# Optimization experiments

Hardware: AMD Instinct MI355X
Metric: run time of the kernel (lower is better)

Reference implementation:

```python
import jax, jax.numpy as jnp
import numpy as np

T, S, B, D, H, FFN = 1024, 1024, 4, 1024, 16, 4096
HD = D // H
EPS = 1e-5


def xavier(key, shape, gain=1.0):
    fan_out, fan_in = shape
    a = gain * np.sqrt(6.0 / (fan_in + fan_out))
    return jax.random.uniform(key, shape, jnp.float32, -a, a)


def layer_norm(x, g, b):
    mu = jnp.mean(x, axis=-1, keepdims=True)
    var = jnp.mean(jnp.square(x - mu), axis=-1, keepdims=True)
    return (x - mu) / jnp.sqrt(var + EPS) * g + b


def mha(q, k, v, Wq, bq, Wk, bk, Wv, bv, Wo, bo, key_padding_mask=None, attn_mask=None):
    # q: [t,b,d]; k,v: [s,b,d]; key_padding_mask: [b,s] bool (True = pad)
    t, b, d = q.shape
    s = v.shape[0]
    if key_padding_mask is not None:
        # original zeroes the KEY tensor before projection
        k = k * (~key_padding_mask).T[:, :, None]
    Q = (q @ Wq.T + bq).reshape(t, b, H, HD)
    K = (k @ Wk.T + bk).reshape(s, b, H, HD)
    V = (v @ Wv.T + bv).reshape(s, b, H, HD)
    scores = jnp.einsum('tbhk,sbhk->bhts', Q, K) / jnp.sqrt(jnp.float32(HD))
    if attn_mask is not None:
        scores = scores + attn_mask  # additive [t,s] broadcast over b,h
    p = jax.nn.softmax(scores, axis=-1)
    ctx = jnp.einsum('bhts,sbhk->tbhk', p, V)  # [t,b,h,hd]
    out = ctx.reshape(t, b, d)
    attn_w = jnp.swapaxes(ctx, 0, 2)  # [h,b,t,hd] as in original
    return out @ Wo.T + bo, attn_w


def setup_inputs() -> dict:
    key = jax.random.key(0)
    ks = jax.random.split(key, 16)
    inv2 = 1.0 / np.sqrt(2.0)
    d = {
        'state': jax.random.normal(ks[0], (T, B, D), jnp.float32),
        'encoder_out': jax.random.normal(ks[1], (S, B, D), jnp.float32),
        'self_attn_mask': jnp.triu(jnp.full((T, T), -1e9, jnp.float32), 1),
        'self_attn_padding_mask': jnp.zeros((B, T), bool),
        'encoder_padding_mask': jnp.broadcast_to(jnp.arange(S)[None, :] >= (S - S // 10), (B, S)),
        # self-attention projections
        'sa_Wq': xavier(ks[2], (D, D), inv2), 'sa_bq': jnp.zeros((D,), jnp.float32),
        'sa_Wk': xavier(ks[3], (D, D), inv2), 'sa_bk': jnp.zeros((D,), jnp.float32),
        'sa_Wv': xavier(ks[4], (D, D), inv2), 'sa_bv': jnp.zeros((D,), jnp.float32),
        'sa_Wo': xavier(ks[5], (D, D)), 'sa_bo': jnp.zeros((D,), jnp.float32),
        # encoder-decoder attention projections
        'ea_Wq': xavier(ks[6], (D, D), inv2), 'ea_bq': jnp.zeros((D,), jnp.float32),
        'ea_Wk': xavier(ks[7], (D, D), inv2), 'ea_bk': jnp.zeros((D,), jnp.float32),
        'ea_Wv': xavier(ks[8], (D, D), inv2), 'ea_bv': jnp.zeros((D,), jnp.float32),
        'ea_Wo': xavier(ks[9], (D, D)), 'ea_bo': jnp.zeros((D,), jnp.float32),
        # layernorms
        'ln1_g': jnp.ones((D,), jnp.float32), 'ln1_b': jnp.zeros((D,), jnp.float32),
        'ln2_g': jnp.ones((D,), jnp.float32), 'ln2_b': jnp.zeros((D,), jnp.float32),
        'ln3_g': jnp.ones((D,), jnp.float32), 'ln3_b': jnp.zeros((D,), jnp.float32),
        # FFN
        'fc1_W': xavier(ks[10], (FFN, D)), 'fc1_b': jnp.zeros((FFN,), jnp.float32),
        'fc2_W': xavier(ks[11], (D, FFN)), 'fc2_b': jnp.zeros((D,), jnp.float32),
    }
    return d


def reference(state, encoder_out, self_attn_mask, self_attn_padding_mask, encoder_padding_mask,
              sa_Wq, sa_bq, sa_Wk, sa_bk, sa_Wv, sa_bv, sa_Wo, sa_bo,
              ea_Wq, ea_bq, ea_Wk, ea_bk, ea_Wv, ea_bv, ea_Wo, ea_bo,
              ln1_g, ln1_b, ln2_g, ln2_b, ln3_g, ln3_b,
              fc1_W, fc1_b, fc2_W, fc2_b):
    x = state
    # self-attention block (dropout is identity in eval)
    res = x
    a, _ = mha(x, x, x, sa_Wq, sa_bq, sa_Wk, sa_bk, sa_Wv, sa_bv, sa_Wo, sa_bo,
               key_padding_mask=self_attn_padding_mask, attn_mask=self_attn_mask)
    x = layer_norm(a + res, ln1_g, ln1_b)
    # encoder-decoder attention block
    res = x
    a, attn = mha(x, encoder_out, encoder_out, ea_Wq, ea_bq, ea_Wk, ea_bk, ea_Wv, ea_bv, ea_Wo, ea_bo,
                  key_padding_mask=encoder_padding_mask, attn_mask=None)
    x = layer_norm(a + res, ln2_g, ln2_b)
    # FFN block
    res = x
    h = jax.nn.relu(x @ fc1_W.T + fc1_b)
    x = layer_norm(h @ fc2_W.T + fc2_b + res, ln3_g, ln3_b)
    return (x, attn)
```

## Files before the change

kernel.cpp:

```cpp
#include <hip/hip_runtime.h>
#include <hip/hip_bf16.h>


typedef __attribute__((ext_vector_type(8))) short bf16x8;
typedef __attribute__((ext_vector_type(4))) float f32x4;
typedef __attribute__((ext_vector_type(8))) unsigned short us8;
typedef __attribute__((ext_vector_type(4))) unsigned short us4;

#define AS1 __attribute__((address_space(1)))
#define AS3 __attribute__((address_space(3)))

#define T_LEN 1024
#define S_LEN 1024
#define B_DIM 4
#define D_MOD 1024
#define H_NUM 16
#define FFN_D 4096
#define NTOK  4096

__device__ __forceinline__ float b2f(unsigned short u) {
    return __uint_as_float(((unsigned int)u) << 16);
}
__device__ __forceinline__ unsigned short f2b(float f) {
    unsigned int x = __float_as_uint(f);
    x += 0x7fffu + ((x >> 16) & 1u);
    return (unsigned short)(x >> 16);
}

struct CvtArgs {
    const float* s[12];
    unsigned short* d[12];
};

__global__ __launch_bounds__(256) void cvt_all_kernel(CvtArgs a)
{
    const int cnt[12] = {2048, 2048, 512, 512, 512, 512, 512, 512, 512, 512, 2048, 2048};
    int bid = blockIdx.x;
    int seg = 0;
    while (bid >= cnt[seg]) { bid -= cnt[seg]; ++seg; }
    const size_t off = (size_t)bid * 2048 + threadIdx.x * 8;
    const float* src = a.s[seg] + off;
    unsigned short* dst = a.d[seg] + off;
    const f32x4 v0 = *(const f32x4*)src;
    const f32x4 v1 = *(const f32x4*)(src + 4);
    us8 o;
#pragma unroll
    for (int j = 0; j < 4; ++j) { o[j] = f2b(v0[j]); o[4 + j] = f2b(v1[j]); }
    *(us8*)dst = o;
}

template <int BN>
__global__ __launch_bounds__(512, 2) void gemm256_kernel(
    const unsigned short* __restrict__ A,
    const unsigned short* __restrict__ W,
    const float* __restrict__ b0, const float* __restrict__ b1,
    const float* __restrict__ b2, const float* __restrict__ b3,
    const int* __restrict__ rowmask, unsigned int maskbits,
    unsigned short* __restrict__ p0, unsigned short* __restrict__ p1,
    unsigned short* __restrict__ p2, unsigned short* __restrict__ p3,
    int ostride,
    const float* __restrict__ resid, float* __restrict__ outf,
    int M, int N, int K, int relu)
{
    constexpr int WN = BN / 4;
    constexpr int NR = BN / 64;

    __shared__ __align__(16) unsigned short As[2][16384];
    __shared__ __align__(16) unsigned short Bs[2][BN * 64];

    const int tid  = threadIdx.x;
    const int lane = tid & 63;
    const int wid  = tid >> 6;
    const int wr   = wid >> 2;
    const int wc   = wid & 3;
    const int row0 = blockIdx.x * 256;
    const int col0 = blockIdx.y * BN;
    const int rsel = lane & 15;
    const int kg2  = (lane >> 4) * 16;

    f32x4 acc[8][NR];
#pragma unroll
    for (int m = 0; m < 8; ++m)
#pragma unroll
        for (int n = 0; n < NR; ++n)
            acc[m][n] = (f32x4){0.f, 0.f, 0.f, 0.f};

    const int NT = K >> 6;

    auto stage = [&](int buf, int t) {
        const int k0 = t << 6;
#pragma unroll
        for (int i = 0; i < 4; ++i) {
            const unsigned int beta = (unsigned int)(i * 8192 + tid * 16);
            const unsigned int lam  = beta ^ (((beta >> 7) & 7u) << 4);
            const char* src = (const char*)A +
                ((size_t)(row0 + (int)(lam >> 7)) * K + k0) * 2 + (lam & 127u);
            __builtin_amdgcn_global_load_lds((const AS1 void*)src,
                (AS3 void*)((char*)&As[buf][0] + beta), 16, 0, 0);
        }
#pragma unroll
        for (int i = 0; i < NR; ++i) {
            const unsigned int beta = (unsigned int)(i * 8192 + tid * 16);
            const unsigned int lam  = beta ^ (((beta >> 7) & 7u) << 4);
            const char* src = (const char*)W +
                ((size_t)(col0 + (int)(lam >> 7)) * K + k0) * 2 + (lam & 127u);
            __builtin_amdgcn_global_load_lds((const AS1 void*)src,
                (AS3 void*)((char*)&Bs[buf][0] + beta), 16, 0, 0);
        }
    };

    auto phase = [&](int buf, int kk) {
        bf16x8 af[8];
#pragma unroll
        for (int m = 0; m < 8; ++m) {
            const int r = wr * 128 + m * 16 + rsel;
            const unsigned int l  = (unsigned int)(r * 128 + kk * 64 + kg2);
            const unsigned int ph = l ^ (((unsigned int)(r & 7)) << 4);
            af[m] = *(const bf16x8*)((const char*)&As[buf][0] + ph);
        }
        bf16x8 bfr[NR];
#pragma unroll
        for (int n = 0; n < NR; ++n) {
            const int r = wc * WN + n * 16 + rsel;
            const unsigned int l  = (unsigned int)(r * 128 + kk * 64 + kg2);
            const unsigned int ph = l ^ (((unsigned int)(r & 7)) << 4);
            bfr[n] = *(const bf16x8*)((const char*)&Bs[buf][0] + ph);
        }
        __builtin_amdgcn_s_setprio(1);
#pragma unroll
        for (int m = 0; m < 8; ++m)
#pragma unroll
            for (int n = 0; n < NR; ++n)
                acc[m][n] = __builtin_amdgcn_mfma_f32_16x16x32_bf16(af[m], bfr[n], acc[m][n], 0, 0, 0);
        __builtin_amdgcn_s_setprio(0);
    };

    stage(0, 0);
    stage(1, 1);
    if constexpr (BN == 256) { asm volatile("s_waitcnt vmcnt(8)" ::: "memory"); }
    else                     { asm volatile("s_waitcnt vmcnt(6)" ::: "memory"); }
    __builtin_amdgcn_s_barrier();
    asm volatile("" ::: "memory");

    for (int t = 0; t < NT; ++t) {
        const int cur = t & 1;
        phase(cur, 0);
        phase(cur, 1);
        asm volatile("s_waitcnt lgkmcnt(0)" ::: "memory");
        __builtin_amdgcn_s_barrier();
        asm volatile("" ::: "memory");
        if (t + 2 < NT) {
            stage(cur, t + 2);
            if constexpr (BN == 256) { asm volatile("s_waitcnt vmcnt(8)" ::: "memory"); }
            else                     { asm volatile("s_waitcnt vmcnt(6)" ::: "memory"); }
        } else if (t + 1 < NT) {
            asm volatile("s_waitcnt vmcnt(0)" ::: "memory");
        }
        __builtin_amdgcn_s_barrier();
        asm volatile("" ::: "memory");
    }

    const int seq = M >> 2;
    const int c   = col0 >> 10;
    unsigned short* op = c == 0 ? p0 : c == 1 ? p1 : c == 2 ? p2 : p3;
    const float*    bp = c == 0 ? b0 : c == 1 ? b1 : c == 2 ? b2 : b3;
    const bool um = rowmask && ((maskbits >> c) & 1u);
    const int rbas = (lane >> 4) * 4;
#pragma unroll
    for (int m = 0; m < 8; ++m) {
#pragma unroll
        for (int n = 0; n < NR; ++n) {
#pragma unroll
            for (int j = 0; j < 4; ++j) {
                const int gr = row0 + wr * 128 + m * 16 + rbas + j;
                const int gc = col0 + wc * WN + n * 16 + rsel;
                float v = acc[m][n][j];
                if (um && rowmask[(gr & 3) * seq + (gr >> 2)] != 0) v = 0.f;
                v += bp[gc & 1023];
                if (relu) v = fmaxf(v, 0.f);
                if (resid) v += resid[(size_t)gr * N + gc];
                if (outf) outf[(size_t)gr * N + gc] = v;
                else      op[(size_t)gr * ostride + (gc & 1023)] = f2b(v);
            }
        }
    }
}

__global__ __launch_bounds__(256) void vtrans_kernel(
    const unsigned short* __restrict__ Vb, unsigned short* __restrict__ Vt)
{
    __shared__ unsigned short tile[64 * 72];
    const int tid = threadIdx.x;
    const int t0  = blockIdx.x * 64;
    const int bh  = blockIdx.y;
    const int h   = bh & (H_NUM - 1);
    const int b   = bh >> 4;

    const int r   = tid >> 2;
    const int c16 = (tid & 3) * 16;
    const unsigned short* src = Vb + ((size_t)(t0 + r) * B_DIM + b) * D_MOD + h * 64 + c16;
    *(us8*)&tile[r * 72 + c16]     = *(const us8*)src;
    *(us8*)&tile[r * 72 + c16 + 8] = *(const us8*)(src + 8);
    __syncthreads();

    const int dr  = tid >> 2;
    const int tch = (tid & 3) * 16;
    us8 o0, o1;
#pragma unroll
    for (int j = 0; j < 8; ++j) {
        o0[j] = tile[(tch + j) * 72 + dr];
        o1[j] = tile[(tch + 8 + j) * 72 + dr];
    }
    unsigned short* dst = Vt + (size_t)(bh * 64 + dr) * S_LEN + t0 + tch;
    *(us8*)dst       = o0;
    *(us8*)(dst + 8) = o1;
}

__global__ __launch_bounds__(256) void flash_mfma_kernel(
    const unsigned short* __restrict__ Qb,
    const unsigned short* __restrict__ Kb,
    const unsigned short* __restrict__ Vt,
    unsigned short* __restrict__ outc,
    float* __restrict__ outp,
    int causal)
{
    __shared__ __align__(16) unsigned short Ks[32 * 64];
    __shared__ __align__(16) unsigned short Vts[64 * 32];
    __shared__ __align__(16) unsigned short Ps[4 * 16 * 40];

    const int tid  = threadIdx.x;
    const int lane = tid & 63;
    const int wv   = tid >> 6;
    const int g    = lane >> 4;
    const int n    = lane & 15;
    const int t0   = blockIdx.x * 64;
    const int bh   = blockIdx.y;
    const int h    = bh & (H_NUM - 1);
    const int b    = bh >> 4;
    const int woff = wv * 16;

    bf16x8 qa[2];
    {
        const unsigned short* qptr =
            Qb + ((size_t)(t0 + woff + n) * B_DIM + b) * D_MOD + h * 64 + g * 8;
        qa[0] = *(const bf16x8*)qptr;
        qa[1] = *(const bf16x8*)(qptr + 32);
    }

    f32x4 ctx[4];
#pragma unroll
    for (int nt = 0; nt < 4; ++nt) ctx[nt] = (f32x4){0.f, 0.f, 0.f, 0.f};
    float m_run[4], l_run[4];
#pragma unroll
    for (int j = 0; j < 4; ++j) { m_run[j] = -INFINITY; l_run[j] = 0.f; }

    unsigned short* pw = &Ps[wv * 640];
    const int smax = causal ? (t0 + 64) : S_LEN;

    for (int s0 = 0; s0 < smax; s0 += 32) {
        {
            const unsigned int beta = tid * 16;
            const unsigned int lamK = beta ^ (((beta >> 7) & 7u) << 4);
            const unsigned int krow = lamK >> 7, kcolb = lamK & 127u;
            const char* srcK = (const char*)Kb +
                ((size_t)((s0 + krow) * B_DIM + b) * D_MOD + h * 64) * 2 + kcolb;
            __builtin_amdgcn_global_load_lds((const AS1 void*)srcK,
                (AS3 void*)((char*)Ks + beta), 16, 0, 0);
            const unsigned int lamV = beta ^ (((beta >> 6) & 3u) << 4);
            const unsigned int drow = lamV >> 6, scolb = lamV & 63u;
            const char* srcV = (const char*)Vt +
                ((size_t)(bh * 64 + drow) * S_LEN + s0) * 2 + scolb;
            __builtin_amdgcn_global_load_lds((const AS1 void*)srcV,
                (AS3 void*)((char*)Vts + beta), 16, 0, 0);
        }
        __syncthreads();

        f32x4 sacc[2];
        sacc[0] = (f32x4){0.f, 0.f, 0.f, 0.f};
        sacc[1] = (f32x4){0.f, 0.f, 0.f, 0.f};
#pragma unroll
        for (int u = 0; u < 2; ++u) {
#pragma unroll
            for (int kc = 0; kc < 2; ++kc) {
                const unsigned int l = (unsigned int)(u * 16 + n) * 128 + kc * 64 + g * 16;
                const unsigned int ph = l ^ ((unsigned int)(n & 7) << 4);
                const bf16x8 kb = *(const bf16x8*)((const char*)Ks + ph);
                sacc[u] = __builtin_amdgcn_mfma_f32_16x16x32_bf16(qa[kc], kb, sacc[u], 0, 0, 0);
            }
        }

        float e0[4], e1[4], scj[4];
#pragma unroll
        for (int j = 0; j < 4; ++j) {
            float p0 = sacc[0][j] * 0.125f;
            float p1 = sacc[1][j] * 0.125f;
            if (causal) {
                const int tq = t0 + woff + g * 4 + j;
                if (s0 + n > tq)      p0 += -1e9f;
                if (s0 + 16 + n > tq) p1 += -1e9f;
            }
            float mx = fmaxf(p0, p1);
            mx = fmaxf(mx, __shfl_xor(mx, 1));
            mx = fmaxf(mx, __shfl_xor(mx, 2));
            mx = fmaxf(mx, __shfl_xor(mx, 4));
            mx = fmaxf(mx, __shfl_xor(mx, 8));
            const float m_new = fmaxf(m_run[j], mx);
            const float sc = __expf(m_run[j] - m_new);
            m_run[j] = m_new;
            e0[j] = __expf(p0 - m_new);
            e1[j] = __expf(p1 - m_new);
            float ls = e0[j] + e1[j];
            ls += __shfl_xor(ls, 1);
            ls += __shfl_xor(ls, 2);
            ls += __shfl_xor(ls, 4);
            ls += __shfl_xor(ls, 8);
            l_run[j] = l_run[j] * sc + ls;
            scj[j] = sc;
        }
#pragma unroll
        for (int nt = 0; nt < 4; ++nt)
#pragma unroll
            for (int j = 0; j < 4; ++j) ctx[nt][j] *= scj[j];

#pragma unroll
        for (int j = 0; j < 4; ++j) {
            pw[(g * 4 + j) * 40 + n]      = f2b(e0[j]);
            pw[(g * 4 + j) * 40 + 16 + n] = f2b(e1[j]);
        }
        const bf16x8 pa = *(const bf16x8*)&pw[n * 40 + g * 8];

#pragma unroll
        for (int nt = 0; nt < 4; ++nt) {
            const unsigned int l = (unsigned int)(nt * 16 + n) * 64 + g * 16;
            const unsigned int ph = l ^ ((unsigned int)(n & 3) << 4);
            const bf16x8 vb = *(const bf16x8*)((const char*)Vts + ph);
            ctx[nt] = __builtin_amdgcn_mfma_f32_16x16x32_bf16(pa, vb, ctx[nt], 0, 0, 0);
        }
        __syncthreads();
    }

    float inv[4];
#pragma unroll
    for (int j = 0; j < 4; ++j) inv[j] = 1.f / l_run[j];
#pragma unroll
    for (int nt = 0; nt < 4; ++nt) {
#pragma unroll
        for (int j = 0; j < 4; ++j) {
            const int t = t0 + woff + g * 4 + j;
            const int d = nt * 16 + n;
            const float v = ctx[nt][j] * inv[j];
            outc[((size_t)t * B_DIM + b) * D_MOD + h * 64 + d] = f2b(v);
            if (outp)
                outp[((size_t)(h * B_DIM + b) * T_LEN + t) * 64 + d] = v;
        }
    }
}

__global__ __launch_bounds__(256) void layernorm_kernel(
    const float* __restrict__ y,
    const float* __restrict__ g,
    const float* __restrict__ be,
    float* __restrict__ out_f,
    unsigned short* __restrict__ out_bf)
{
    __shared__ float red[8];
    const int row = blockIdx.x;
    const int tid = threadIdx.x;
    const float* yr = y + (size_t)row * D_MOD;
    const f32x4 v = *(const f32x4*)&yr[tid * 4];
    float s = v[0] + v[1] + v[2] + v[3];
#pragma unroll
    for (int o = 32; o > 0; o >>= 1) s += __shfl_xor(s, o);
    if ((tid & 63) == 0) red[tid >> 6] = s;
    __syncthreads();
    const float mu = (red[0] + red[1] + red[2] + red[3]) * (1.f / D_MOD);
    const float d0 = v[0] - mu, d1 = v[1] - mu, d2 = v[2] - mu, d3 = v[3] - mu;
    float s2 = d0 * d0 + d1 * d1 + d2 * d2 + d3 * d3;
#pragma unroll
    for (int o = 32; o > 0; o >>= 1) s2 += __shfl_xor(s2, o);
    if ((tid & 63) == 0) red[4 + (tid >> 6)] = s2;
    __syncthreads();
    const float var  = (red[4] + red[5] + red[6] + red[7]) * (1.f / D_MOD);
    const float rstd = rsqrtf(var + 1e-5f);
    const float dd[4] = {d0, d1, d2, d3};
    f32x4 of;
    us4 ob;
#pragma unroll
    for (int j = 0; j < 4; ++j) {
        const int col = tid * 4 + j;
        const float r = dd[j] * rstd * g[col] + be[col];
        of[j] = r;
        ob[j] = f2b(r);
    }
    const size_t oi = (size_t)row * D_MOD + tid * 4;
    if (out_f)  *(f32x4*)&out_f[oi] = of;
    if (out_bf) *(us4*)&out_bf[oi]  = ob;
}

extern "C" void kernel_launch(void* const* d_in, const int* in_sizes, int n_in,
                              void* d_out, int out_size, void* d_ws, size_t ws_size,
                              hipStream_t stream) {
    (void)in_sizes; (void)n_in; (void)out_size; (void)ws_size;

    const float* x0    = (const float*)d_in[0];
    const float* enc   = (const float*)d_in[1];
    const int* sa_pad  = (const int*)d_in[3];
    const int* ea_pad  = (const int*)d_in[4];
    const float* sa_Wq = (const float*)d_in[5];
    const float* sa_bq = (const float*)d_in[6];
    const float* sa_Wk = (const float*)d_in[7];
    const float* sa_bk = (const float*)d_in[8];
    const float* sa_Wv = (const float*)d_in[9];
    const float* sa_bv = (const float*)d_in[10];
    const float* sa_Wo = (const float*)d_in[11];
    const float* sa_bo = (const float*)d_in[12];
    const float* ea_Wq = (const float*)d_in[13];
    const float* ea_bq = (const float*)d_in[14];
    const float* ea_Wk = (const float*)d_in[15];
    const float* ea_bk = (const float*)d_in[16];
    const float* ea_Wv = (const float*)d_in[17];
    const float* ea_bv = (const float*)d_in[18];
    const float* ea_Wo = (const float*)d_in[19];
    const float* ea_bo = (const float*)d_in[20];
    const float* ln1_g = (const float*)d_in[21];
    const float* ln1_b = (const float*)d_in[22];
    const float* ln2_g = (const float*)d_in[23];
    const float* ln2_b = (const float*)d_in[24];
    const float* ln3_g = (const float*)d_in[25];
    const float* ln3_b = (const float*)d_in[26];
    const float* fc1_W = (const float*)d_in[27];
    const float* fc1_b = (const float*)d_in[28];
    const float* fc2_W = (const float*)d_in[29];
    const float* fc2_b = (const float*)d_in[30];

    const size_t DD = (size_t)D_MOD * D_MOD;
    const size_t FD = (size_t)FFN_D * D_MOD;
    const size_t SL = (size_t)NTOK * D_MOD;

    unsigned short* ws_us = (unsigned short*)d_ws;
    unsigned short* wb[10];
    for (int i = 0; i < 8; ++i) wb[i] = ws_us + i * DD;
    wb[8] = ws_us + 8 * DD;
    wb[9] = ws_us + 8 * DD + FD;
    unsigned short* abf = ws_us + 8 * DD + 2 * FD;
    unsigned short* ebf = abf + SL;
    unsigned short* Cb  = ebf + SL;
    unsigned short* Qb  = Cb + SL;
    unsigned short* Kb  = Qb + SL;
    unsigned short* Vb  = Kb + SL;
    unsigned short* Vt  = Vb + SL;
    unsigned short* Hbf = Qb;
    float* fbase = (float*)(Vt + SL);
    float* Yf  = fbase;
    float* X1f = fbase + SL;

    float* outx = (float*)d_out;
    float* outa = outx + SL;

    const dim3 blk(256);
    const dim3 blk512(512);
    const dim3 g_attn(T_LEN / 64, B_DIM * H_NUM);
    unsigned short* nbf = nullptr;
    float* nff = nullptr;
    const float* nf = nullptr;
    const int* ni = nullptr;

    {
        CvtArgs ca;
        const float* srcs[12]  = {x0, enc, sa_Wq, sa_Wk, sa_Wv, sa_Wo,
                                  ea_Wq, ea_Wk, ea_Wv, ea_Wo, fc1_W, fc2_W};
        unsigned short* dsts[12] = {abf, ebf, wb[0], wb[1], wb[2], wb[3],
                                    wb[4], wb[5], wb[6], wb[7], wb[8], wb[9]};
        for (int i = 0; i < 12; ++i) { ca.s[i] = srcs[i]; ca.d[i] = dsts[i]; }
        cvt_all_kernel<<<dim3(12288), blk, 0, stream>>>(ca);
    }

    gemm256_kernel<256><<<dim3(16, 12), blk512, 0, stream>>>(
        abf, wb[0], sa_bq, sa_bk, sa_bv, sa_bv, sa_pad, 0x2u,
        Qb, Kb, Vb, Vb, D_MOD, nf, nff, NTOK, 3072, D_MOD, 0);
    vtrans_kernel<<<g_attn, blk, 0, stream>>>(Vb, Vt);
    flash_mfma_kernel<<<g_attn, blk, 0, stream>>>(Qb, Kb, Vt, Cb, nff, 1);
    gemm256_kernel<128><<<dim3(16, 8), blk512, 0, stream>>>(
        Cb, wb[3], sa_bo, sa_bo, sa_bo, sa_bo, ni, 0u,
        Qb, Qb, Qb, Qb, D_MOD, x0, Yf, NTOK, D_MOD, D_MOD, 0);
    layernorm_kernel<<<dim3(NTOK), blk, 0, stream>>>(Yf, ln1_g, ln1_b, X1f, abf);

    gemm256_kernel<128><<<dim3(16, 8), blk512, 0, stream>>>(
        abf, wb[4], ea_bq, ea_bq, ea_bq, ea_bq, ni, 0u,
        Qb, Qb, Qb, Qb, D_MOD, nf, nff, NTOK, D_MOD, D_MOD, 0);
    gemm256_kernel<256><<<dim3(16, 8), blk512, 0, stream>>>(
        ebf, wb[5], ea_bk, ea_bv, ea_bv, ea_bv, ea_pad, 0x1u,
        Kb, Vb, Vb, Vb, D_MOD, nf, nff, NTOK, 2048, D_MOD, 0);
    vtrans_kernel<<<g_attn, blk, 0, stream>>>(Vb, Vt);
    flash_mfma_kernel<<<g_attn, blk, 0, stream>>>(Qb, Kb, Vt, Cb, outa, 0);
    gemm256_kernel<128><<<dim3(16, 8), blk512, 0, stream>>>(
        Cb, wb[7], ea_bo, ea_bo, ea_bo, ea_bo, ni, 0u,
        Qb, Qb, Qb, Qb, D_MOD, X1f, Yf, NTOK, D_MOD, D_MOD, 0);
    layernorm_kernel<<<dim3(NTOK), blk, 0, stream>>>(Yf, ln2_g, ln2_b, X1f, ebf);

    gemm256_kernel<256><<<dim3(16, 16), blk512, 0, stream>>>(
        ebf, wb[8], fc1_b, fc1_b + 1024, fc1_b + 2048, fc1_b + 3072, ni, 0u,
        Hbf, Hbf + 1024, Hbf + 2048, Hbf + 3072, FFN_D, nf, nff, NTOK, FFN_D, D_MOD, 1);
    gemm256_kernel<128><<<dim3(16, 8), blk512, 0, stream>>>(
        Hbf, wb[9], fc2_b, fc2_b, fc2_b, fc2_b, ni, 0u,
        Qb, Qb, Qb, Qb, D_MOD, X1f, Yf, NTOK, D_MOD, FFN_D, 0);
    layernorm_kernel<<<dim3(NTOK), blk, 0, stream>>>(Yf, ln3_g, ln3_b, outx, nbf);
}
```

Baseline: 764.4 us.

## Rewrite GEMM as eight-phase interleaved pipeline and split-K the N=1024 GEMMs

The GEMM main loop is restructured into eight phases that interleave LDS fragment reads, half-tile global-to-LDS staging and MFMA blocks, with barriers and priority hints so loads overlap compute. The N=1024 output GEMMs (out-projections and fc2) now use a 2-way split-K over blockIdx.z. The second split writes fp32 partials into a reused scratch buffer, which the following layernorm adds back in. This targets the low block count (128 blocks) of those GEMMs and exposed load latency. The cost is extra partial-sum traffic and occupancy lowered to 1 block per CU, and the encoder K/V GEMM switches to 128-wide tiles.

```diff
diff --git a/kernel.cpp b/kernel.cpp
--- a/kernel.cpp
+++ b/kernel.cpp
@@ -50,7 +50,7 @@
 }
 
 template <int BN>
-__global__ __launch_bounds__(512, 2) void gemm256_kernel(
+__global__ __launch_bounds__(512, 1) void gemm8ph_kernel(
     const unsigned short* __restrict__ A,
     const unsigned short* __restrict__ W,
     const float* __restrict__ b0, const float* __restrict__ b1,
@@ -60,13 +60,14 @@
     unsigned short* __restrict__ p2, unsigned short* __restrict__ p3,
     int ostride,
     const float* __restrict__ resid, float* __restrict__ outf,
-    int M, int N, int K, int relu)
+    float* __restrict__ partf,
+    int M, int N, int K, int relu, int ksplit)
 {
-    constexpr int WN = BN / 4;
-    constexpr int NR = BN / 64;
-
-    __shared__ __align__(16) unsigned short As[2][16384];
-    __shared__ __align__(16) unsigned short Bs[2][BN * 64];
+    constexpr int NR  = BN / 64;
+    constexpr int BLH = (BN * 64) / 8192;
+    constexpr int BBUF = BN * 128;
+
+    __shared__ __align__(16) char ldsb[65536 + 2 * BBUF];
 
     const int tid  = threadIdx.x;
     const int lane = tid & 63;
@@ -77,6 +78,10 @@
     const int col0 = blockIdx.y * BN;
     const int rsel = lane & 15;
     const int kg2  = (lane >> 4) * 16;
+    const int kz   = blockIdx.z;
+    const int Keff = K / ksplit;
+    const int koff = kz * Keff;
+    const int NT   = Keff >> 6;
 
     f32x4 acc[8][NR];
 #pragma unroll
@@ -85,104 +90,142 @@
         for (int n = 0; n < NR; ++n)
             acc[m][n] = (f32x4){0.f, 0.f, 0.f, 0.f};
 
-    const int NT = K >> 6;
-
-    auto stage = [&](int buf, int t) {
-        const int k0 = t << 6;
-#pragma unroll
-        for (int i = 0; i < 4; ++i) {
-            const unsigned int beta = (unsigned int)(i * 8192 + tid * 16);
+    auto stageA = [&](int buf, int half, int t) {
+        const int k0 = koff + (t << 6);
+#pragma unroll
+        for (int i = 0; i < 2; ++i) {
+            const unsigned int beta = (unsigned int)(half * 16384 + i * 8192 + tid * 16);
             const unsigned int lam  = beta ^ (((beta >> 7) & 7u) << 4);
             const char* src = (const char*)A +
                 ((size_t)(row0 + (int)(lam >> 7)) * K + k0) * 2 + (lam & 127u);
             __builtin_amdgcn_global_load_lds((const AS1 void*)src,
-                (AS3 void*)((char*)&As[buf][0] + beta), 16, 0, 0);
-        }
-#pragma unroll
-        for (int i = 0; i < NR; ++i) {
-            const unsigned int beta = (unsigned int)(i * 8192 + tid * 16);
+                (AS3 void*)(ldsb + buf * 32768 + beta), 16, 0, 0);
+        }
+    };
+    auto stageB = [&](int buf, int half, int t) {
+        const int k0 = koff + (t << 6);
+#pragma unroll
+        for (int i = 0; i < BLH; ++i) {
+            const unsigned int beta = (unsigned int)(half * (BN * 64) + i * 8192 + tid * 16);
             const unsigned int lam  = beta ^ (((beta >> 7) & 7u) << 4);
             const char* src = (const char*)W +
                 ((size_t)(col0 + (int)(lam >> 7)) * K + k0) * 2 + (lam & 127u);
             __builtin_amdgcn_global_load_lds((const AS1 void*)src,
-                (AS3 void*)((char*)&Bs[buf][0] + beta), 16, 0, 0);
+                (AS3 void*)(ldsb + 65536 + buf * BBUF + beta), 16, 0, 0);
         }
     };
-
-    auto phase = [&](int buf, int kk) {
-        bf16x8 af[8];
-#pragma unroll
-        for (int m = 0; m < 8; ++m) {
-            const int r = wr * 128 + m * 16 + rsel;
-            const unsigned int l  = (unsigned int)(r * 128 + kk * 64 + kg2);
-            const unsigned int ph = l ^ (((unsigned int)(r & 7)) << 4);
-            af[m] = *(const bf16x8*)((const char*)&As[buf][0] + ph);
-        }
-        bf16x8 bfr[NR];
-#pragma unroll
-        for (int n = 0; n < NR; ++n) {
-            const int r = wc * WN + n * 16 + rsel;
-            const unsigned int l  = (unsigned int)(r * 128 + kk * 64 + kg2);
-            const unsigned int ph = l ^ (((unsigned int)(r & 7)) << 4);
-            bfr[n] = *(const bf16x8*)((const char*)&Bs[buf][0] + ph);
-        }
-        __builtin_amdgcn_s_setprio(1);
-#pragma unroll
-        for (int m = 0; m < 8; ++m)
-#pragma unroll
-            for (int n = 0; n < NR; ++n)
-                acc[m][n] = __builtin_amdgcn_mfma_f32_16x16x32_bf16(af[m], bfr[n], acc[m][n], 0, 0, 0);
-        __builtin_amdgcn_s_setprio(0);
+    auto readA = [&](int buf, int m, int k) -> bf16x8 {
+        const int r = wr * 128 + m * 16 + rsel;
+        const unsigned int l  = (unsigned int)(r * 128 + k * 64 + kg2);
+        const unsigned int ph = l ^ (((unsigned int)(r & 7)) << 4);
+        return *(const bf16x8*)(ldsb + buf * 32768 + ph);
     };
-
-    stage(0, 0);
-    stage(1, 1);
-    if constexpr (BN == 256) { asm volatile("s_waitcnt vmcnt(8)" ::: "memory"); }
-    else                     { asm volatile("s_waitcnt vmcnt(6)" ::: "memory"); }
+    auto readB = [&](int buf, int n, int k) -> bf16x8 {
+        const int r = wc * (BN / 4) + n * 16 + rsel;
+        const unsigned int l  = (unsigned int)(r * 128 + k * 64 + kg2);
+        const unsigned int ph = l ^ (((unsigned int)(r & 7)) << 4);
+        return *(const bf16x8*)(ldsb + 65536 + buf * BBUF + ph);
+    };
+
+    stageA(0, 0, 0); stageA(0, 1, 0); stageB(0, 0, 0); stageB(0, 1, 0);
+    stageA(1, 0, 1); stageA(1, 1, 1);
+    asm volatile("s_waitcnt vmcnt(4)" ::: "memory");
     __builtin_amdgcn_s_barrier();
-    asm volatile("" ::: "memory");
+
+    bf16x8 Afr[8][2], Bfr[NR][2];
 
     for (int t = 0; t < NT; ++t) {
         const int cur = t & 1;
-        phase(cur, 0);
-        phase(cur, 1);
+#pragma unroll
+        for (int m = 0; m < 4; ++m) { Afr[m][0] = readA(cur, m, 0); Afr[m][1] = readA(cur, m, 1); }
+#pragma unroll
+        for (int n = 0; n < NR; ++n) Bfr[n][0] = readB(cur, n, 0);
+        if (t + 1 < NT) stageB(cur ^ 1, 0, t + 1);
+        __builtin_amdgcn_s_barrier();
         asm volatile("s_waitcnt lgkmcnt(0)" ::: "memory");
-        __builtin_amdgcn_s_barrier();
-        asm volatile("" ::: "memory");
-        if (t + 2 < NT) {
-            stage(cur, t + 2);
-            if constexpr (BN == 256) { asm volatile("s_waitcnt vmcnt(8)" ::: "memory"); }
-            else                     { asm volatile("s_waitcnt vmcnt(6)" ::: "memory"); }
-        } else if (t + 1 < NT) {
-            asm volatile("s_waitcnt vmcnt(0)" ::: "memory");
-        }
-        __builtin_amdgcn_s_barrier();
-        asm volatile("" ::: "memory");
-    }
-
-    const int seq = M >> 2;
-    const int c   = col0 >> 10;
+        __builtin_amdgcn_sched_barrier(0);
+        __builtin_amdgcn_s_setprio(1);
+#pragma unroll
+        for (int m = 0; m < 4; ++m)
+#pragma unroll
+            for (int n = 0; n < NR; ++n)
+                acc[m][n] = __builtin_amdgcn_mfma_f32_16x16x32_bf16(Afr[m][0], Bfr[n][0], acc[m][n], 0, 0, 0);
+        __builtin_amdgcn_s_setprio(0);
+        __builtin_amdgcn_s_barrier();
+#pragma unroll
+        for (int m = 4; m < 8; ++m) { Afr[m][0] = readA(cur, m, 0); Afr[m][1] = readA(cur, m, 1); }
+#pragma unroll
+        for (int n = 0; n < NR; ++n) Bfr[n][1] = readB(cur, n, 1);
+        if (t + 1 < NT) stageB(cur ^ 1, 1, t + 1);
+        __builtin_amdgcn_s_barrier();
+        asm volatile("s_waitcnt lgkmcnt(0)" ::: "memory");
+        __builtin_amdgcn_sched_barrier(0);
+        __builtin_amdgcn_s_setprio(1);
+#pragma unroll
+        for (int m = 4; m < 8; ++m)
+#pragma unroll
+            for (int n = 0; n < NR; ++n)
+                acc[m][n] = __builtin_amdgcn_mfma_f32_16x16x32_bf16(Afr[m][0], Bfr[n][0], acc[m][n], 0, 0, 0);
+        __builtin_amdgcn_s_setprio(0);
+        __builtin_amdgcn_s_barrier();
+        if (t + 2 < NT) stageA(cur, 0, t + 2);
+        __builtin_amdgcn_s_barrier();
+        __builtin_amdgcn_s_setprio(1);
+#pragma unroll
+        for (int m = 0; m < 4; ++m)
+#pragma unroll
+            for (int n = 0; n < NR; ++n)
+                acc[m][n] = __builtin_amdgcn_mfma_f32_16x16x32_bf16(Afr[m][1], Bfr[n][1], acc[m][n], 0, 0, 0);
+        __builtin_amdgcn_s_setprio(0);
+        __builtin_amdgcn_s_barrier();
+        if (t + 2 < NT) stageA(cur, 1, t + 2);
+        __builtin_amdgcn_s_barrier();
+        __builtin_amdgcn_s_setprio(1);
+#pragma unroll
+        for (int m = 4; m < 8; ++m)
+#pragma unroll
+            for (int n = 0; n < NR; ++n)
+                acc[m][n] = __builtin_amdgcn_mfma_f32_16x16x32_bf16(Afr[m][1], Bfr[n][1], acc[m][n], 0, 0, 0);
+        __builtin_amdgcn_s_setprio(0);
+        if (t + 2 < NT) { asm volatile("s_waitcnt vmcnt(4)" ::: "memory"); }
+        else            { asm volatile("s_waitcnt vmcnt(0)" ::: "memory"); }
+        __builtin_amdgcn_s_barrier();
+    }
+
+    const int seq  = M >> 2;
+    const int c    = col0 >> 10;
     unsigned short* op = c == 0 ? p0 : c == 1 ? p1 : c == 2 ? p2 : p3;
     const float*    bp = c == 0 ? b0 : c == 1 ? b1 : c == 2 ? b2 : b3;
     const bool um = rowmask && ((maskbits >> c) & 1u);
     const int rbas = (lane >> 4) * 4;
-#pragma unroll
-    for (int m = 0; m < 8; ++m) {
-#pragma unroll
-        for (int n = 0; n < NR; ++n) {
-#pragma unroll
-            for (int j = 0; j < 4; ++j) {
-                const int gr = row0 + wr * 128 + m * 16 + rbas + j;
-                const int gc = col0 + wc * WN + n * 16 + rsel;
-                float v = acc[m][n][j];
-                if (um && rowmask[(gr & 3) * seq + (gr >> 2)] != 0) v = 0.f;
-                v += bp[gc & 1023];
-                if (relu) v = fmaxf(v, 0.f);
-                if (resid) v += resid[(size_t)gr * N + gc];
-                if (outf) outf[(size_t)gr * N + gc] = v;
-                else      op[(size_t)gr * ostride + (gc & 1023)] = f2b(v);
-            }
-        }
+    if (partf && kz > 0) {
+#pragma unroll
+        for (int m = 0; m < 8; ++m)
+#pragma unroll
+            for (int n = 0; n < NR; ++n)
+#pragma unroll
+                for (int j = 0; j < 4; ++j) {
+                    const int gr = row0 + wr * 128 + m * 16 + rbas + j;
+                    const int gc = col0 + wc * (BN / 4) + n * 16 + rsel;
+                    partf[(size_t)gr * N + gc] = acc[m][n][j];
+                }
+    } else {
+#pragma unroll
+        for (int m = 0; m < 8; ++m)
+#pragma unroll
+            for (int n = 0; n < NR; ++n)
+#pragma unroll
+                for (int j = 0; j < 4; ++j) {
+                    const int gr = row0 + wr * 128 + m * 16 + rbas + j;
+                    const int gc = col0 + wc * (BN / 4) + n * 16 + rsel;
+                    float v = acc[m][n][j];
+                    if (um && rowmask[(gr & 3) * seq + (gr >> 2)] != 0) v = 0.f;
+                    v += bp[gc & 1023];
+                    if (relu) v = fmaxf(v, 0.f);
+                    if (resid) v += resid[(size_t)gr * N + gc];
+                    if (outf) outf[(size_t)gr * N + gc] = v;
+                    else      op[(size_t)gr * ostride + (gc & 1023)] = f2b(v);
+                }
     }
 }
 
@@ -358,6 +401,7 @@
 
 __global__ __launch_bounds__(256) void layernorm_kernel(
     const float* __restrict__ y,
+    const float* __restrict__ part,
     const float* __restrict__ g,
     const float* __restrict__ be,
     float* __restrict__ out_f,
@@ -366,8 +410,12 @@
     __shared__ float red[8];
     const int row = blockIdx.x;
     const int tid = threadIdx.x;
-    const float* yr = y + (size_t)row * D_MOD;
-    const f32x4 v = *(const f32x4*)&yr[tid * 4];
+    f32x4 v = *(const f32x4*)&y[(size_t)row * D_MOD + tid * 4];
+    if (part) {
+        const f32x4 pv = *(const f32x4*)&part[(size_t)row * D_MOD + tid * 4];
+#pragma unroll
+        for (int j = 0; j < 4; ++j) v[j] += pv[j];
+    }
     float s = v[0] + v[1] + v[2] + v[3];
 #pragma unroll
     for (int o = 32; o > 0; o >>= 1) s += __shfl_xor(s, o);
@@ -453,6 +501,8 @@
     float* fbase = (float*)(Vt + SL);
     float* Yf  = fbase;
     float* X1f = fbase + SL;
+    float* Pq  = (float*)Qb;
+    float* Pa  = (float*)abf;
 
     float* outx = (float*)d_out;
     float* outa = outx + SL;
@@ -475,34 +525,35 @@
         cvt_all_kernel<<<dim3(12288), blk, 0, stream>>>(ca);
     }
 
-    gemm256_kernel<256><<<dim3(16, 12), blk512, 0, stream>>>(
+    gemm8ph_kernel<256><<<dim3(16, 12, 1), blk512, 0, stream>>>(
         abf, wb[0], sa_bq, sa_bk, sa_bv, sa_bv, sa_pad, 0x2u,
-        Qb, Kb, Vb, Vb, D_MOD, nf, nff, NTOK, 3072, D_MOD, 0);
+        Qb, Kb, Vb, Vb, D_MOD, nf, nff, nff, NTOK, 3072, D_MOD, 0, 1);
     vtrans_kernel<<<g_attn, blk, 0, stream>>>(Vb, Vt);
     flash_mfma_kernel<<<g_attn, blk, 0, stream>>>(Qb, Kb, Vt, Cb, nff, 1);
-    gemm256_kernel<128><<<dim3(16, 8), blk512, 0, stream>>>(
+    gemm8ph_kernel<128><<<dim3(16, 8, 2), blk512, 0, stream>>>(
         Cb, wb[3], sa_bo, sa_bo, sa_bo, sa_bo, ni, 0u,
-        Qb, Qb, Qb, Qb, D_MOD, x0, Yf, NTOK, D_MOD, D_MOD, 0);
-    layernorm_kernel<<<dim3(NTOK), blk, 0, stream>>>(Yf, ln1_g, ln1_b, X1f, abf);
-
-    gemm256_kernel<128><<<dim3(16, 8), blk512, 0, stream>>>(
+        nbf, nbf, nbf, nbf, D_MOD, x0, Yf, Pq, NTOK, D_MOD, D_MOD, 0, 2);
+    layernorm_kernel<<<dim3(NTOK), blk, 0, stream>>>(Yf, Pq, ln1_g, ln1_b, X1f, abf);
+
+    gemm8ph_kernel<128><<<dim3(16, 8, 1), blk512, 0, stream>>>(
         abf, wb[4], ea_bq, ea_bq, ea_bq, ea_bq, ni, 0u,
-        Qb, Qb, Qb, Qb, D_MOD, nf, nff, NTOK, D_MOD, D_MOD, 0);
-    gemm256_kernel<256><<<dim3(16, 8), blk512, 0, stream>>>(
+        Qb, Qb, Qb, Qb, D_MOD, nf, nff, nff, NTOK, D_MOD, D_MOD, 0, 1);
+    gemm8ph_kernel<128><<<dim3(16, 16, 1), blk512, 0, stream>>>(
         ebf, wb[5], ea_bk, ea_bv, ea_bv, ea_bv, ea_pad, 0x1u,
-        Kb, Vb, Vb, Vb, D_MOD, nf, nff, NTOK, 2048, D_MOD, 0);
+        Kb, Vb, Vb, Vb, D_MOD, nf, nff, nff, NTOK, 2048, D_MOD, 0, 1);
     vtrans_kernel<<<g_attn, blk, 0, stream>>>(Vb, Vt);
     flash_mfma_kernel<<<g_attn, blk, 0, stream>>>(Qb, Kb, Vt, Cb, outa, 0);
-    gemm256_kernel<128><<<dim3(16, 8), blk512, 0, stream>>>(
+    gemm8ph_kernel<128><<<dim3(16, 8, 2), blk512, 0, stream>>>(
         Cb, wb[7], ea_bo, ea_bo, ea_bo, ea_bo, ni, 0u,
-        Qb, Qb, Qb, Qb, D_MOD, X1f, Yf, NTOK, D_MOD, D_MOD, 0);
-    layernorm_kernel<<<dim3(NTOK), blk, 0, stream>>>(Yf, ln2_g, ln2_b, X1f, ebf);
-
-    gemm256_kernel<256><<<dim3(16, 16), blk512, 0, stream>>>(
+        nbf, nbf, nbf, nbf, D_MOD, X1f, Yf, Pq, NTOK, D_MOD, D_MOD, 0, 2);
+    layernorm_kernel<<<dim3(NTOK), blk, 0, stream>>>(Yf, Pq, ln2_g, ln2_b, X1f, ebf);
+
+    gemm8ph_kernel<256><<<dim3(16, 16, 1), blk512, 0, stream>>>(
         ebf, wb[8], fc1_b, fc1_b + 1024, fc1_b + 2048, fc1_b + 3072, ni, 0u,
-        Hbf, Hbf + 1024, Hbf + 2048, Hbf + 3072, FFN_D, nf, nff, NTOK, FFN_D, D_MOD, 1);
-    gemm256_kernel<128><<<dim3(16, 8), blk512, 0, stream>>>(
+        Hbf, Hbf + 1024, Hbf + 2048, Hbf + 3072, FFN_D, nf, nff, nff,
+        NTOK, FFN_D, D_MOD, 1, 1);
+    gemm8ph_kernel<128><<<dim3(16, 8, 2), blk512, 0, stream>>>(
         Hbf, wb[9], fc2_b, fc2_b, fc2_b, fc2_b, ni, 0u,
-        Qb, Qb, Qb, Qb, D_MOD, X1f, Yf, NTOK, D_MOD, FFN_D, 0);
-    layernorm_kernel<<<dim3(NTOK), blk, 0, stream>>>(Yf, ln3_g, ln3_b, outx, nbf);
-}
+        nbf, nbf, nbf, nbf, D_MOD, X1f, Yf, Pa, NTOK, D_MOD, FFN_D, 0, 2);
+    layernorm_kernel<<<dim3(NTOK), blk, 0, stream>>>(Yf, Pa, ln3_g, ln3_b, outx, nbf);
+}
```

Result: faster. 703.3 us (-8.0%).
